# Optimization experiments

Measured on AMD Instinct MI355X. Metric: run time of the kernel, lower is better.

Reference implementation:

```python
import jax, jax.numpy as jnp
import numpy as np

N_NODES = 27
SRC = jnp.array([0,1,1,1,1,2,2,2,3,3,3,4,4,4,5,5,5,5,6,6,6,6,6,7,7,7,8,8,8,9,9,9,10,10,10,11,11,11,12,12,12,13,13,13,14,14,14,15,15,15,16,16,16,17,17,17,18,18,18,18,19,20,21,21,21,22,23,23,23,24,25,26], dtype=jnp.int32)
DST = jnp.array([1,0,2,4,6,1,3,7,2,4,24,1,3,5,4,6,17,19,1,5,7,8,10,2,6,23,6,9,16,8,10,13,6,9,11,10,12,23,11,13,21,9,12,14,13,15,20,14,16,18,8,15,17,5,16,18,15,17,25,26,5,14,12,22,23,21,7,11,21,3,18,18], dtype=jnp.int32)


def _conv2d(x, w, b):
    # x: [BN, Cin, H, W], w: [Cout, Cin, 3, 3] -> SAME padding conv
    y = jax.lax.conv_general_dilated(x, w, window_strides=(1, 1), padding='SAME',
                                     dimension_numbers=('NCHW', 'OIHW', 'NCHW'))
    return y + b[None, :, None, None]


def _block(h, w, b):
    # h: [B, N, Cin, H, W]; Conv2dMessage (conv -> scatter-add over edges) + LeakyReLU(0.2) + MaxPool2d(2)
    B, N, C, H, W = h.shape
    y = _conv2d(h.reshape(B * N, C, H, W), w, b).reshape(B, N, -1, H, W)
    # propagate with aggr='add': out[dst] += y[src]; isolated-in nodes become zero
    agg = jnp.zeros_like(y).at[:, DST].add(y[:, SRC])
    a = jax.nn.leaky_relu(agg, negative_slope=0.2)
    Co = a.shape[2]
    p = jax.lax.reduce_window(a.reshape(B * N, Co, H, W), -jnp.inf, jax.lax.max,
                              (1, 1, 2, 2), (1, 1, 2, 2), 'VALID')
    return p.reshape(B, N, Co, H // 2, W // 2)


def setup_inputs() -> dict:
    key = jax.random.key(0)
    ks = jax.random.split(key, 9)
    B, Cin, H, W = 32, 4, 64, 64
    x = jax.random.normal(ks[0], (B, Cin, H, W), dtype=jnp.float32)
    def kaiming(k, shape):
        fan_in = int(np.prod(shape[1:]))
        bound = float(np.sqrt(6.0 / fan_in))
        return jax.random.uniform(k, shape, jnp.float32, -bound, bound)
    w1 = kaiming(ks[1], (32, Cin, 3, 3)); b1 = jnp.zeros((32,), jnp.float32)
    w2 = kaiming(ks[2], (64, 32, 3, 3));  b2 = jnp.zeros((64,), jnp.float32)
    w3 = kaiming(ks[3], (128, 64, 3, 3)); b3 = jnp.zeros((128,), jnp.float32)
    wc = kaiming(ks[4], (1, 128));        bc = jnp.zeros((1,), jnp.float32)
    return {"x": x, "w1": w1, "b1": b1, "w2": w2, "b2": b2,
            "w3": w3, "b3": b3, "wc": wc, "bc": bc}


def reference(x, w1, b1, w2, b2, w3, b3, wc, bc):
    B = x.shape[0]
    # torch.tile(xi, (27,1,1,1)) vectorized over batch -> [B, 27, C, H, W]
    h = jnp.broadcast_to(x[:, None], (B, N_NODES) + x.shape[1:])
    h = _block(h, w1, b1)   # [B, 27, 32, 32, 32]
    h = _block(h, w2, b2)   # [B, 27, 64, 16, 16]
    h = _block(h, w3, b3)   # [B, 27, 128, 8, 8]
    feat = h.mean(axis=(3, 4))                 # AdaptiveAvgPool2d(1) + flatten -> [B, 27, 128]
    logits = jnp.einsum('bnc,oc->bno', feat, wc) + bc  # [B, 27, 1]
    return logits[:, 0, :]                     # classifier(xi)[0] per sample -> [B, 1]
```

## Files before the change

### kernel.cpp

```cpp
#include <hip/hip_runtime.h>


#define LRELU(v) fmaxf((v), 0.2f * (v))

#define P1H_ELEMS (32 * 32 * 34 * 36)
#define P2H_ELEMS (32 * 64 * 18 * 20)

__global__ __launch_bounds__(256, 4) void k1(const float* __restrict__ x,
                                             const float* __restrict__ w1,
                                             const float* __restrict__ b1,
                                             float* __restrict__ P1H,
                                             float* __restrict__ out) {
    __shared__ __align__(16) float obuf[1152];
    const int bx = blockIdx.x;
    const int b  = blockIdx.y;
    const int rb = bx & 3, cog = bx >> 2;
    const int t  = threadIdx.x;
    const int l = t & 63, wv = t >> 6;
    const int r = l >> 4, q = l & 15;
    const int row0 = 16 * rb + 4 * wv + r;

    if (bx == 0 && t == 0) out[b] = 0.f;

    for (int i = t; i < 288; i += 256)
        *(float4*)&obuf[4 * i] = make_float4(0.f, 0.f, 0.f, 0.f);
    __syncthreads();

    const bool cL = (q > 0), cR = (q < 15);
    const int colL = max(4 * q - 2, 0);
    const int colR = min(4 * q + 4, 62);

    float acc[4][4];
    #pragma unroll
    for (int g = 0; g < 4; ++g) {
        float bias = b1[cog * 4 + g];
        acc[g][0] = bias; acc[g][1] = bias; acc[g][2] = bias; acc[g][3] = bias;
    }

    #pragma unroll
    for (int c = 0; c < 4; ++c) {
        float win[3][6];
        #pragma unroll
        for (int d = 0; d < 3; ++d) {
            int gr = row0 - 1 + d;
            bool v = (unsigned)gr < 64u;
            int grc = min(max(gr, 0), 63);
            const float* row = x + ((b * 4 + c) * 64 + grc) * 64;
            float2 L  = *(const float2*)(row + colL);
            float4 M  = *(const float4*)(row + 4 * q);
            float2 R2 = *(const float2*)(row + colR);
            win[d][0] = (v && cL) ? L.y : 0.f;
            win[d][1] = v ? M.x : 0.f;
            win[d][2] = v ? M.y : 0.f;
            win[d][3] = v ? M.z : 0.f;
            win[d][4] = v ? M.w : 0.f;
            win[d][5] = (v && cR) ? R2.x : 0.f;
        }
        #pragma unroll
        for (int g = 0; g < 4; ++g) {
            const float* wp = &w1[((cog * 4 + g) * 4 + c) * 9];
            #pragma unroll
            for (int d = 0; d < 3; ++d)
                #pragma unroll
                for (int j = 0; j < 3; ++j) {
                    float w = wp[3 * d + j];
                    acc[g][0] += w * win[d][j];
                    acc[g][1] += w * win[d][j + 1];
                    acc[g][2] += w * win[d][j + 2];
                    acc[g][3] += w * win[d][j + 3];
                }
        }
    }

    const int prow_l = 2 * wv + (r >> 1);
    #pragma unroll
    for (int g = 0; g < 4; ++g) {
        float m0 = fmaxf(LRELU(acc[g][0]), LRELU(acc[g][1]));
        float m1 = fmaxf(LRELU(acc[g][2]), LRELU(acc[g][3]));
        float p0 = fmaxf(m0, __shfl_xor(m0, 16));
        float p1 = fmaxf(m1, __shfl_xor(m1, 16));
        if ((r & 1) == 0) {
            obuf[(g * 8 + prow_l) * 36 + 2 * q + 1] = 12.f * p0;
            obuf[(g * 8 + prow_l) * 36 + 2 * q + 2] = 12.f * p1;
        }
    }
    __syncthreads();

    for (int i = t; i < 288; i += 256) {
        int co_l = i / 72, rem = i % 72, pr = rem / 9, cw = rem % 9;
        *(float4*)&P1H[((b * 32 + cog * 4 + co_l) * 34 + 8 * rb + pr + 1) * 36 + 4 * cw] =
            *(const float4*)&obuf[4 * i];
    }
    if (rb == 0 || rb == 3) {
        int h = rb ? 33 : 0;
        for (int i = t; i < 36; i += 256) {
            int co_l = i / 9, cw = i % 9;
            *(float4*)&P1H[((b * 32 + cog * 4 + co_l) * 34 + h) * 36 + 4 * cw] =
                make_float4(0.f, 0.f, 0.f, 0.f);
        }
    }
}

__global__ __launch_bounds__(256, 4) void k2(const float* __restrict__ P1H,
                                             const float* __restrict__ w2,
                                             const float* __restrict__ b2,
                                             float* __restrict__ p2H) {
    __shared__ __align__(16) float xin[6912];
    __shared__ __align__(16) float obuf[640];
    const int bx = blockIdx.x;
    const int b  = blockIdx.y;
    const int cog = bx >> 3, rs = bx & 7;
    const int c0  = cog * 16;
    const int t = threadIdx.x, l = t & 63;
    const int wvs = __builtin_amdgcn_readfirstlane(t >> 6);
    const int ql = l & 15, R = l >> 4;

    for (int i = t; i < 1728; i += 256) {
        int cin = i / 54, rem = i % 54, r = rem / 9, cw = rem % 9;
        *(float4*)&xin[cin * 216 + r * 36 + 4 * cw] =
            *(const float4*)&P1H[((b * 32 + cin) * 34 + rs * 4 + r) * 36 + 4 * cw];
    }
    for (int i = t; i < 160; i += 256)
        *(float4*)&obuf[4 * i] = make_float4(0.f, 0.f, 0.f, 0.f);
    __syncthreads();

    float acc[16][2];
    #pragma unroll
    for (int co = 0; co < 16; ++co) {
        float bias = (wvs == 0) ? 4.f * b2[c0 + co] : 0.f;
        acc[co][0] = bias; acc[co][1] = bias;
    }

    #pragma unroll 2
    for (int cl = 0; cl < 8; ++cl) {
        const int cin = wvs * 8 + cl;
        float win[3][4];
        #pragma unroll
        for (int d = 0; d < 3; ++d) {
            const float* xr = &xin[cin * 216 + (R + d) * 36 + 2 * ql];
            float2 a0 = *(const float2*)xr;
            float2 a1 = *(const float2*)(xr + 2);
            win[d][0] = a0.x; win[d][1] = a0.y; win[d][2] = a1.x; win[d][3] = a1.y;
        }
        const int wbase = __builtin_amdgcn_readfirstlane((c0 * 32 + cin) * 9);
        #pragma unroll
        for (int co = 0; co < 16; ++co) {
            const float* wg = w2 + wbase + co * 288;
            float wt[9];
            #pragma unroll
            for (int k = 0; k < 9; ++k) wt[k] = wg[k];
            #pragma unroll
            for (int d = 0; d < 3; ++d)
                #pragma unroll
                for (int j = 0; j < 3; ++j) {
                    float w = wt[3 * d + j];
                    acc[co][0] += w * win[d][j];
                    acc[co][1] += w * win[d][j + 1];
                }
        }
    }

    __syncthreads();
    if (wvs > 0) {
        float* cb = &xin[((wvs - 1) * 64 + l) * 36];
        #pragma unroll
        for (int g = 0; g < 8; ++g)
            *(float4*)&cb[4 * g] = make_float4(acc[2 * g][0], acc[2 * g][1],
                                               acc[2 * g + 1][0], acc[2 * g + 1][1]);
    }
    __syncthreads();
    if (wvs == 0) {
        #pragma unroll
        for (int k = 0; k < 3; ++k) {
            const float* cb = &xin[(k * 64 + l) * 36];
            #pragma unroll
            for (int g = 0; g < 8; ++g) {
                float4 v = *(const float4*)&cb[4 * g];
                acc[2 * g][0] += v.x; acc[2 * g][1] += v.y;
                acc[2 * g + 1][0] += v.z; acc[2 * g + 1][1] += v.w;
            }
        }
        #pragma unroll
        for (int co = 0; co < 16; ++co) {
            float m = fmaxf(LRELU(acc[co][0]), LRELU(acc[co][1]));
            float p = fmaxf(m, __shfl_xor(m, 16));
            if ((R & 1) == 0)
                obuf[(co * 2 + (R >> 1)) * 20 + ql + 1] = p;
        }
    }
    __syncthreads();

    for (int i = t; i < 160; i += 256) {
        int co = i / 10, rem = i % 10, pr = rem / 5, cw = rem % 5;
        *(float4*)&p2H[((b * 64 + c0 + co) * 18 + rs * 2 + 1 + pr) * 20 + 4 * cw] =
            *(const float4*)&obuf[4 * i];
    }
    if (rs == 0 || rs == 7) {
        int h2 = rs ? 17 : 0;
        for (int i = t; i < 80; i += 256) {
            int co = i / 5, cw = i % 5;
            *(float4*)&p2H[((b * 64 + c0 + co) * 18 + h2) * 20 + 4 * cw] =
                make_float4(0.f, 0.f, 0.f, 0.f);
        }
    }
}

__global__ __launch_bounds__(256, 4) void k3(const float* __restrict__ p2H,
                                             const float* __restrict__ w3,
                                             const float* __restrict__ b3,
                                             const float* __restrict__ wc,
                                             const float* __restrict__ bc,
                                             float* __restrict__ out) {
    __shared__ __align__(16) float cbuf[3840];
    const int cog = blockIdx.x;
    const int b   = blockIdx.y;
    const int c0  = cog * 4;
    const int t   = threadIdx.x, l = t & 63;
    const int wvs = __builtin_amdgcn_readfirstlane(t >> 6);
    const int r   = l >> 2, q = l & 3;

    float acc[4][4];
    #pragma unroll
    for (int g = 0; g < 4; ++g) {
        float bias = (wvs == 0) ? b3[c0 + g] : 0.f;
        acc[g][0] = bias; acc[g][1] = bias; acc[g][2] = bias; acc[g][3] = bias;
    }

    #pragma unroll 4
    for (int cl = 0; cl < 16; ++cl) {
        const int cin = wvs * 16 + cl;
        const float* pb = p2H + (((b * 64 + cin) * 18 + r) * 20 + 4 * q);
        float win[3][6];
        #pragma unroll
        for (int d = 0; d < 3; ++d) {
            float4 M  = *(const float4*)(pb + d * 20);
            float2 Rt = *(const float2*)(pb + d * 20 + 4);
            win[d][0] = M.x; win[d][1] = M.y; win[d][2] = M.z;
            win[d][3] = M.w; win[d][4] = Rt.x; win[d][5] = Rt.y;
        }
        const int wbase = __builtin_amdgcn_readfirstlane((c0 * 64 + cin) * 9);
        #pragma unroll
        for (int g = 0; g < 4; ++g) {
            const float* wg = w3 + wbase + g * 576;
            float wt[9];
            #pragma unroll
            for (int k = 0; k < 9; ++k) wt[k] = wg[k];
            #pragma unroll
            for (int d = 0; d < 3; ++d)
                #pragma unroll
                for (int j = 0; j < 3; ++j) {
                    float w = wt[3 * d + j];
                    acc[g][0] += w * win[d][j];
                    acc[g][1] += w * win[d][j + 1];
                    acc[g][2] += w * win[d][j + 2];
                    acc[g][3] += w * win[d][j + 3];
                }
        }
    }

    if (wvs > 0) {
        float* cb = &cbuf[((wvs - 1) * 64 + l) * 20];
        #pragma unroll
        for (int g = 0; g < 4; ++g)
            *(float4*)&cb[4 * g] =
                make_float4(acc[g][0], acc[g][1], acc[g][2], acc[g][3]);
    }
    __syncthreads();

    if (wvs == 0) {
        #pragma unroll
        for (int k = 0; k < 3; ++k) {
            const float* cb = &cbuf[(k * 64 + l) * 20];
            #pragma unroll
            for (int g = 0; g < 4; ++g) {
                float4 v = *(const float4*)&cb[4 * g];
                acc[g][0] += v.x; acc[g][1] += v.y;
                acc[g][2] += v.z; acc[g][3] += v.w;
            }
        }
        float vsum = 0.f;
        #pragma unroll
        for (int g = 0; g < 4; ++g) {
            float m0 = fmaxf(LRELU(acc[g][0]), LRELU(acc[g][1]));
            float m1 = fmaxf(LRELU(acc[g][2]), LRELU(acc[g][3]));
            float pm0 = fmaxf(m0, __shfl_xor(m0, 4));
            float pm1 = fmaxf(m1, __shfl_xor(m1, 4));
            float contrib = ((r & 1) == 0) ? (pm0 + pm1) : 0.f;
            vsum += contrib * wc[c0 + g];
        }
        #pragma unroll
        for (int off = 32; off > 0; off >>= 1) vsum += __shfl_xor(vsum, off);
        if (l == 0) {
            float o = vsum * (1.f / 64.f);
            if (cog == 0) o += bc[0];
            atomicAdd(&out[b], o);
        }
    }
}

extern "C" void kernel_launch(void* const* d_in, const int* in_sizes, int n_in,
                              void* d_out, int out_size, void* d_ws, size_t ws_size,
                              hipStream_t stream) {
    const float* x  = (const float*)d_in[0];
    const float* w1 = (const float*)d_in[1];
    const float* b1 = (const float*)d_in[2];
    const float* w2 = (const float*)d_in[3];
    const float* b2 = (const float*)d_in[4];
    const float* w3 = (const float*)d_in[5];
    const float* b3 = (const float*)d_in[6];
    const float* wc = (const float*)d_in[7];
    const float* bc = (const float*)d_in[8];
    float* out = (float*)d_out;

    float* P1H = (float*)d_ws;
    float* p2H = P1H + P1H_ELEMS;

    k1<<<dim3(32, 32), 256, 0, stream>>>(x, w1, b1, P1H, out);
    k2<<<dim3(32, 32), 256, 0, stream>>>(P1H, w2, b2, p2H);
    k3<<<dim3(32, 32), 256, 0, stream>>>(p2H, w3, b3, wc, bc, out);
}
```

Before: 131.2 us.

## Fuse three conv stages into one cooperative kernel with grid syncs

Merges the three per-layer kernels into a single cooperative kernel of 1024 blocks that runs each phase in turn, with a grid-wide barrier between phases. Shared memory becomes one buffer sized for the largest phase. The aim is to remove the launch gaps and tail drain between separate kernel launches. The cost is two grid barriers, higher shared-memory use in phases 1 and 3, and a fallback to the three old launches if the cooperative launch fails (for example, if all 1024 blocks cannot be co-resident).

```diff
diff --git a/kernel.cpp b/kernel.cpp
--- a/kernel.cpp
+++ b/kernel.cpp
@@ -1,4 +1,7 @@
 #include <hip/hip_runtime.h>
+#include <hip/hip_cooperative_groups.h>
+
+namespace cg = cooperative_groups;
 
 
 #define LRELU(v) fmaxf((v), 0.2f * (v))
@@ -6,14 +9,13 @@
 #define P1H_ELEMS (32 * 32 * 34 * 36)
 #define P2H_ELEMS (32 * 64 * 18 * 20)
 
-__global__ __launch_bounds__(256, 4) void k1(const float* __restrict__ x,
-                                             const float* __restrict__ w1,
-                                             const float* __restrict__ b1,
-                                             float* __restrict__ P1H,
-                                             float* __restrict__ out) {
-    __shared__ __align__(16) float obuf[1152];
-    const int bx = blockIdx.x;
-    const int b  = blockIdx.y;
+__device__ __forceinline__ void phase1(const int bx, const int b,
+                                       const float* __restrict__ x,
+                                       const float* __restrict__ w1,
+                                       const float* __restrict__ b1,
+                                       float* __restrict__ P1H,
+                                       float* __restrict__ out,
+                                       float* __restrict__ obuf) {
     const int rb = bx & 3, cog = bx >> 2;
     const int t  = threadIdx.x;
     const int l = t & 63, wv = t >> 6;
@@ -101,14 +103,14 @@
     }
 }
 
-__global__ __launch_bounds__(256, 4) void k2(const float* __restrict__ P1H,
-                                             const float* __restrict__ w2,
-                                             const float* __restrict__ b2,
-                                             float* __restrict__ p2H) {
-    __shared__ __align__(16) float xin[6912];
-    __shared__ __align__(16) float obuf[640];
-    const int bx = blockIdx.x;
-    const int b  = blockIdx.y;
+__device__ __forceinline__ void phase2(const int bx, const int b,
+                                       const float* __restrict__ P1H,
+                                       const float* __restrict__ w2,
+                                       const float* __restrict__ b2,
+                                       float* __restrict__ p2H,
+                                       float* __restrict__ smem) {
+    float* xin  = smem;
+    float* obuf = smem + 6912;
     const int cog = bx >> 3, rs = bx & 7;
     const int c0  = cog * 16;
     const int t = threadIdx.x, l = t & 63;
@@ -205,15 +207,14 @@
     }
 }
 
-__global__ __launch_bounds__(256, 4) void k3(const float* __restrict__ p2H,
-                                             const float* __restrict__ w3,
-                                             const float* __restrict__ b3,
-                                             const float* __restrict__ wc,
-                                             const float* __restrict__ bc,
-                                             float* __restrict__ out) {
-    __shared__ __align__(16) float cbuf[3840];
-    const int cog = blockIdx.x;
-    const int b   = blockIdx.y;
+__device__ __forceinline__ void phase3(const int cog, const int b,
+                                       const float* __restrict__ p2H,
+                                       const float* __restrict__ w3,
+                                       const float* __restrict__ b3,
+                                       const float* __restrict__ wc,
+                                       const float* __restrict__ bc,
+                                       float* __restrict__ out,
+                                       float* __restrict__ cbuf) {
     const int c0  = cog * 4;
     const int t   = threadIdx.x, l = t & 63;
     const int wvs = __builtin_amdgcn_readfirstlane(t >> 6);
@@ -296,6 +297,57 @@
             atomicAdd(&out[b], o);
         }
     }
+}
+
+__global__ __launch_bounds__(256, 4) void fused(const float* __restrict__ x,
+                                                const float* __restrict__ w1,
+                                                const float* __restrict__ b1,
+                                                const float* __restrict__ w2,
+                                                const float* __restrict__ b2,
+                                                const float* __restrict__ w3,
+                                                const float* __restrict__ b3,
+                                                const float* __restrict__ wc,
+                                                const float* __restrict__ bc,
+                                                float* __restrict__ P1H,
+                                                float* __restrict__ p2H,
+                                                float* __restrict__ out) {
+    __shared__ __align__(16) float smem[7552];
+    const int bid = blockIdx.x;
+    const int b   = bid >> 5;
+    const int bx  = bid & 31;
+
+    phase1(bx, b, x, w1, b1, P1H, out, smem);
+    cg::this_grid().sync();
+    phase2(bx, b, P1H, w2, b2, p2H, smem);
+    cg::this_grid().sync();
+    phase3(bx, b, p2H, w3, b3, wc, bc, out, smem);
+}
+
+__global__ __launch_bounds__(256, 4) void k1(const float* __restrict__ x,
+                                             const float* __restrict__ w1,
+                                             const float* __restrict__ b1,
+                                             float* __restrict__ P1H,
+                                             float* __restrict__ out) {
+    __shared__ __align__(16) float obuf[1152];
+    phase1(blockIdx.x, blockIdx.y, x, w1, b1, P1H, out, obuf);
+}
+
+__global__ __launch_bounds__(256, 4) void k2(const float* __restrict__ P1H,
+                                             const float* __restrict__ w2,
+                                             const float* __restrict__ b2,
+                                             float* __restrict__ p2H) {
+    __shared__ __align__(16) float smem[7552];
+    phase2(blockIdx.x, blockIdx.y, P1H, w2, b2, p2H, smem);
+}
+
+__global__ __launch_bounds__(256, 4) void k3(const float* __restrict__ p2H,
+                                             const float* __restrict__ w3,
+                                             const float* __restrict__ b3,
+                                             const float* __restrict__ wc,
+                                             const float* __restrict__ bc,
+                                             float* __restrict__ out) {
+    __shared__ __align__(16) float cbuf[3840];
+    phase3(blockIdx.x, blockIdx.y, p2H, w3, b3, wc, bc, out, cbuf);
 }
 
 extern "C" void kernel_launch(void* const* d_in, const int* in_sizes, int n_in,
@@ -315,7 +367,14 @@
     float* P1H = (float*)d_ws;
     float* p2H = P1H + P1H_ELEMS;
 
-    k1<<<dim3(32, 32), 256, 0, stream>>>(x, w1, b1, P1H, out);
-    k2<<<dim3(32, 32), 256, 0, stream>>>(P1H, w2, b2, p2H);
-    k3<<<dim3(32, 32), 256, 0, stream>>>(p2H, w3, b3, wc, bc, out);
-}
+    void* args[] = {(void*)&x,  (void*)&w1, (void*)&b1, (void*)&w2, (void*)&b2,
+                    (void*)&w3, (void*)&b3, (void*)&wc, (void*)&bc,
+                    (void*)&P1H, (void*)&p2H, (void*)&out};
+    hipError_t e = hipLaunchCooperativeKernel((const void*)fused, dim3(1024),
+                                              dim3(256), args, 0, stream);
+    if (e != hipSuccess) {
+        k1<<<dim3(32, 32), 256, 0, stream>>>(x, w1, b1, P1H, out);
+        k2<<<dim3(32, 32), 256, 0, stream>>>(P1H, w2, b2, p2H);
+        k3<<<dim3(32, 32), 256, 0, stream>>>(p2H, w3, b3, wc, bc, out);
+    }
+}
```

Result: slower. 353.4 us (+169.4%).
